# Optimization experiments

Hardware: AMD Instinct MI355X
Metric: run time of the kernel (lower is better)

## Reference

```python
import jax, jax.numpy as jnp
import numpy as np

B, T, D, H = 2, 2048, 1024, 16
DH = D // H


def setup_inputs() -> dict:
    key = jax.random.key(0)
    ks = jax.random.split(key, 5)
    scale = 1.0 / np.sqrt(D)
    return {
        "x": jax.random.normal(ks[0], (B, T, D), dtype=jnp.float32),
        "Wq": jax.random.normal(ks[1], (D, D), dtype=jnp.float32) * scale,
        "Wk": jax.random.normal(ks[2], (D, D), dtype=jnp.float32) * scale,
        "Wv": jax.random.normal(ks[3], (D, D), dtype=jnp.float32) * scale,
        "Wo": jax.random.normal(ks[4], (D, D), dtype=jnp.float32) * scale,
    }


def _split(y):
    # (B,T,D) -> (B,H,T,DH)
    b, t, _ = y.shape
    return y.reshape(b, t, H, DH).transpose(0, 2, 1, 3)


def reference(x, Wq, Wk, Wv, Wo):
    q = _split(x @ Wq)
    k = _split(x @ Wk)
    v = _split(x @ Wv)
    scores = jnp.einsum("bhqd,bhkd->bhqk", q, k) / jnp.sqrt(jnp.float32(DH))
    t = x.shape[1]
    # additive causal mask: -1e9 above the diagonal (matches band_part logic)
    causal = jnp.tril(jnp.ones((t, t), dtype=jnp.float32))
    scores = scores + (1.0 - causal) * -1e9
    attn = jax.nn.softmax(scores, axis=-1)
    out = jnp.einsum("bhqk,bhkd->bhqd", attn, v)  # (B,H,T,DH)
    out = out.transpose(0, 2, 1, 3).reshape(x.shape[0], t, D)
    return out @ Wo
```

## Files before the change

kernel.cpp:

```cpp
#include <hip/hip_runtime.h>

#define BB 2
#define TT 2048
#define DD 1024
#define HH 16
#define DHD 64
#define MM (BB*TT)

typedef __attribute__((ext_vector_type(8))) short short8;
typedef __attribute__((ext_vector_type(4))) float float4v;
typedef unsigned short u16;

__device__ inline float bf2f(u16 u) {
    union { unsigned int i; float f; } v;
    v.i = ((unsigned int)u) << 16;
    return v.f;
}
__device__ inline u16 f2bf(float f) {
    union { float f; unsigned int i; } v;
    v.f = f;
    unsigned int x = v.i;
    unsigned int r = (x + 0x7fffu + ((x >> 16) & 1u)) >> 16;
    return (u16)r;
}

__global__ __launch_bounds__(256) void prep_k(const float* __restrict__ x,
                                              const float* __restrict__ Wq,
                                              const float* __restrict__ Wk,
                                              const float* __restrict__ Wv,
                                              const float* __restrict__ Wo,
                                              u16* __restrict__ xb,
                                              u16* __restrict__ WT) {
    int tid = threadIdx.x;
    if (blockIdx.z == 4) {
        int bid = blockIdx.y * 32 + blockIdx.x;
#pragma unroll
        for (int k = 0; k < 4; k++) {
            int i = bid * 1024 + k * 256 + tid;
            float4v v = ((const float4v*)x)[i];
            ushort4 o;
            o.x = f2bf(v[0]); o.y = f2bf(v[1]); o.z = f2bf(v[2]); o.w = f2bf(v[3]);
            ((ushort4*)xb)[i] = o;
        }
        return;
    }
    __shared__ u16 t[32][33];
    int wsel = blockIdx.z;
    const float* W = (wsel == 0) ? Wq : (wsel == 1) ? Wk : (wsel == 2) ? Wv : Wo;
    u16* o = WT + (size_t)wsel * DD * DD;
    int k0 = blockIdx.y * 32, n0 = blockIdx.x * 32;
    int tx = tid & 31, ty = tid >> 5;
#pragma unroll
    for (int i = 0; i < 4; i++) {
        int k = ty + i * 8;
        t[k][tx] = f2bf(W[(size_t)(k0 + k) * DD + n0 + tx]);
    }
    __syncthreads();
#pragma unroll
    for (int i = 0; i < 4; i++) {
        int n = ty + i * 8;
        o[(size_t)(n0 + n) * DD + k0 + tx] = t[tx][n];
    }
}

template <int MODE, int TM, int TN, int BK>
__global__ __launch_bounds__(256) void gemm_k(const u16* __restrict__ A,
                                              const u16* __restrict__ WT0,
                                              void* __restrict__ outp) {
    const int K = DD;
    const int MT = TM / 32, NT = TN / 32;
    const int NS = (TM + TN) * (BK / 8) / 256;
    const int CPR = BK / 8;

    int z = blockIdx.z;
    const u16* WT = WT0 + (size_t)z * DD * DD;
    int n0 = blockIdx.x * TN, m0 = blockIdx.y * TM;

    __shared__ u16 S[(TM + TN) * BK];

    int tid = threadIdx.x;
    int lane = tid & 63, w = tid >> 6;
    int wm = (w >> 1) * (TM / 2), wn = (w & 1) * (TN / 2);
    int quad = lane >> 4, l16 = lane & 15;

    const u16* gp[NS];
    u16* lp[NS];
#pragma unroll
    for (int j = 0; j < NS; j++) {
        int cid = tid + j * 256;
        int r = cid / CPR, c = cid % CPR;
        lp[j] = S + r * BK + (c ^ (r & 7)) * 8;
        gp[j] = (r < TM ? A + (size_t)(m0 + r) * K
                        : WT + (size_t)(n0 + r - TM) * K) + c * 8;
    }
    int swz = l16 & 7;

    float4v acc[MT][NT];
#pragma unroll
    for (int i = 0; i < MT; i++)
#pragma unroll
        for (int j = 0; j < NT; j++) acc[i][j] = (float4v)(0.0f);

    short8 pr[NS];
#pragma unroll
    for (int j = 0; j < NS; j++) pr[j] = *(const short8*)gp[j];

    const int NK = K / BK;
#pragma unroll 1
    for (int ki = 0; ki < NK; ki++) {
        __syncthreads();
#pragma unroll
        for (int j = 0; j < NS; j++) *(short8*)lp[j] = pr[j];
        __syncthreads();

        if (ki + 1 < NK) {
            int k0 = (ki + 1) * BK;
#pragma unroll
            for (int j = 0; j < NS; j++) pr[j] = *(const short8*)(gp[j] + k0);
        }

#pragma unroll
        for (int ks = 0; ks < BK / 32; ks++) {
            int cq = ((ks * 4 + quad) ^ swz) * 8;
            short8 a[MT], b[NT];
#pragma unroll
            for (int mt = 0; mt < MT; mt++)
                a[mt] = *(const short8*)&S[(wm + mt * 16 + l16) * BK + cq];
#pragma unroll
            for (int nt = 0; nt < NT; nt++)
                b[nt] = *(const short8*)&S[(TM + wn + nt * 16 + l16) * BK + cq];
#pragma unroll
            for (int mt = 0; mt < MT; mt++)
#pragma unroll
                for (int nt = 0; nt < NT; nt++)
                    acc[mt][nt] = __builtin_amdgcn_mfma_f32_16x16x32_bf16(
                        a[mt], b[nt], acc[mt][nt], 0, 0, 0);
        }
    }

#pragma unroll
    for (int mt = 0; mt < MT; mt++) {
#pragma unroll
        for (int nt = 0; nt < NT; nt++) {
#pragma unroll
            for (int r = 0; r < 4; r++) {
                int m = m0 + wm + mt * 16 + quad * 4 + r;
                int n = n0 + wn + nt * 16 + l16;
                float v = acc[mt][nt][r];
                if constexpr (MODE == 0) {
                    int bb = m >> 11, t = m & 2047;
                    int h = n >> 6, dh = n & 63;
                    size_t idx;
                    if (z == 2)
                        idx = (((size_t)2 * BB * HH + bb * HH + h) * DHD + dh) * TT + t;
                    else
                        idx = (((size_t)z * BB * HH + bb * HH + h) * TT + t) * DHD + dh;
                    ((u16*)outp)[idx] = f2bf(v);
                } else {
                    ((float*)outp)[(size_t)m * DD + n] = v;
                }
            }
        }
    }
}

__global__ __launch_bounds__(512) void attn_k(const u16* __restrict__ QKV,
                                              u16* __restrict__ AO) {
    const u16* Q  = QKV;
    const u16* Kp = QKV + (size_t)MM * DD;
    const u16* Vp = QKV + (size_t)2 * MM * DD;
    int bh = blockIdx.y;
    int tswz = (blockIdx.x + blockIdx.y) & 15;
    int p = (blockIdx.y & 16) ? (15 - tswz) : tswz;
    int qA = p, qB = 31 - p;
    size_t hoff = (size_t)bh * TT * DHD;

    __shared__ u16 Qs[2][64 * 64];
    __shared__ u16 Ks[2][64 * 64];
    __shared__ u16 VTs[2][64 * 64];
    __shared__ u16 Ps[8][16 * 64];

    int tid = threadIdx.x;
    int lane = tid & 63, wv = tid >> 6;
    int g = wv >> 2, w4 = wv & 3;
    int quad = lane >> 4, l16 = lane & 15;

    int sr = tid >> 3, sc = tid & 7;
    int sl = sr * 64 + ((sc ^ (sr & 7)) * 8);
    const u16* gK = Kp + hoff + (size_t)sr * DHD + sc * 8;
    const u16* gV = Vp + hoff + (size_t)sr * TT + sc * 8;

    const float qscale = 0.125f * 1.4426950408889634f;
#pragma unroll
    for (int t = 0; t < 2; t++) {
        int q0 = (t ? qB : qA) * 64;
        short8 v = *(const short8*)(Q + hoff + (size_t)(q0 + sr) * DHD + sc * 8);
        short8 sv;
#pragma unroll
        for (int e = 0; e < 8; e++) sv[e] = (short)f2bf(bf2f((u16)v[e]) * qscale);
        *(short8*)&Qs[t][sl] = sv;
    }

    short8 prK = *(const short8*)gK;
    short8 prV = *(const short8*)gV;

    __syncthreads();
    int cxs = l16 & 7;
    int fr = w4 * 16 + l16;
    short8 aq0 = *(const short8*)&Qs[g][fr * 64 + ((quad ^ cxs) * 8)];
    short8 aq1 = *(const short8*)&Qs[g][fr * 64 + (((4 + quad) ^ cxs) * 8)];

    int myqt = g ? qB : qA;
    int ntile = myqt + 1;
    int NR = qB + 1;

    float4v o[4];
#pragma unroll
    for (int i = 0; i < 4; i++) o[i] = (float4v)(0.0f);
    float lr = 0.0f;

#pragma unroll 1
    for (int jt = 0; jt < NR; jt++) {
        int db = jt & 1;
        *(short8*)&Ks[db][sl]  = prK;
        *(short8*)&VTs[db][sl] = prV;
        __syncthreads();

        if (jt + 1 < NR) {
            size_t nj = (size_t)(jt + 1) * 64;
            prK = *(const short8*)(gK + nj * DHD);
            prV = *(const short8*)(gV + nj);
        }

        if (jt < ntile) {
            float4v s[4];
#pragma unroll
            for (int ct = 0; ct < 4; ct++) {
                int kr = (ct * 16 + l16) * 64;
                short8 ak0 = *(const short8*)&Ks[db][kr + ((quad ^ cxs) * 8)];
                short8 ak1 = *(const short8*)&Ks[db][kr + (((4 + quad) ^ cxs) * 8)];
                float4v sv = (float4v)(0.0f);
                sv = __builtin_amdgcn_mfma_f32_16x16x32_bf16(ak0, aq0, sv, 0, 0, 0);
                sv = __builtin_amdgcn_mfma_f32_16x16x32_bf16(ak1, aq1, sv, 0, 0, 0);
                s[ct] = sv;
            }

            if (jt == myqt) {
                int ql = w4 * 16 + l16;
#pragma unroll
                for (int ct = 0; ct < 4; ct++)
#pragma unroll
                    for (int r = 0; r < 4; r++) {
                        int kvl = ct * 16 + quad * 4 + r;
                        if (kvl > ql) s[ct][r] = -30000.0f;
                    }
            }

#pragma unroll
            for (int ct = 0; ct < 4; ct++) {
                float p0 = __builtin_amdgcn_exp2f(s[ct][0]);
                float p1 = __builtin_amdgcn_exp2f(s[ct][1]);
                float p2 = __builtin_amdgcn_exp2f(s[ct][2]);
                float p3 = __builtin_amdgcn_exp2f(s[ct][3]);
                lr += (p0 + p1) + (p2 + p3);
                union { float f; unsigned u; } c0, c1, c2, c3;
                c0.f = p0; c1.f = p1; c2.f = p2; c3.f = p3;
                ushort4 pw;
                pw.x = (u16)(c0.u >> 16);
                pw.y = (u16)(c1.u >> 16);
                pw.z = (u16)(c2.u >> 16);
                pw.w = (u16)(c3.u >> 16);
                int chnk = (ct * 2 + (quad >> 1)) ^ cxs;
                *(ushort4*)&Ps[wv][l16 * 64 + chnk * 8 + (quad & 1) * 4] = pw;
            }

            short8 ap0 = *(const short8*)&Ps[wv][l16 * 64 + ((quad ^ cxs) * 8)];
            short8 ap1 = *(const short8*)&Ps[wv][l16 * 64 + (((4 + quad) ^ cxs) * 8)];
#pragma unroll
            for (int ct = 0; ct < 4; ct++) {
                int vr = (ct * 16 + l16) * 64;
                short8 bv0 = *(const short8*)&VTs[db][vr + ((quad ^ cxs) * 8)];
                short8 bv1 = *(const short8*)&VTs[db][vr + (((4 + quad) ^ cxs) * 8)];
                o[ct] = __builtin_amdgcn_mfma_f32_16x16x32_bf16(ap0, bv0, o[ct], 0, 0, 0);
                o[ct] = __builtin_amdgcn_mfma_f32_16x16x32_bf16(ap1, bv1, o[ct], 0, 0, 0);
            }
        }
    }

    float rs = lr;
    rs += __shfl_xor(rs, 16);
    rs += __shfl_xor(rs, 32);
    int gbase = lane & 48;
    float rinv[4];
#pragma unroll
    for (int r = 0; r < 4; r++)
        rinv[r] = 1.0f / __shfl(rs, gbase + quad * 4 + r);

    int b = bh >> 4, h = bh & 15;
    int q0 = myqt * 64;
#pragma unroll
    for (int ct = 0; ct < 4; ct++) {
#pragma unroll
        for (int r = 0; r < 4; r++) {
            int q = q0 + w4 * 16 + quad * 4 + r;
            int d = h * 64 + ct * 16 + l16;
            AO[(size_t)(b * TT + q) * DD + d] = f2bf(o[ct][r] * rinv[r]);
        }
    }
}

extern "C" void kernel_launch(void* const* d_in, const int* in_sizes, int n_in,
                              void* d_out, int out_size, void* d_ws, size_t ws_size,
                              hipStream_t stream) {
    const float* x  = (const float*)d_in[0];
    const float* Wq = (const float*)d_in[1];
    const float* Wk = (const float*)d_in[2];
    const float* Wv = (const float*)d_in[3];
    const float* Wo = (const float*)d_in[4];

    u16* xb  = (u16*)d_ws;
    u16* WT  = xb + (size_t)MM * DD;
    u16* QKV = WT + (size_t)4 * DD * DD;
    u16* AO  = QKV + (size_t)3 * MM * DD;
    float* out = (float*)d_out;

    prep_k<<<dim3(32, 32, 5), 256, 0, stream>>>(x, Wq, Wk, Wv, Wo, xb, WT);
    gemm_k<0, 128, 128, 64><<<dim3(DD / 128, MM / 128, 3), 256, 0, stream>>>(xb, WT, QKV);
    attn_k<<<dim3(16, 32), 512, 0, stream>>>(QKV, AO);
    gemm_k<1, 64, 128, 128><<<dim3(DD / 128, MM / 64, 1), 256, 0, stream>>>(AO, WT + (size_t)3 * DD * DD, out);
}
```

Measured before the change: 170.4 us.

## Split KV range across wave groups per query tile instead of pairing query tiles

The attention kernel now gives each block a single 64-row query tile. Its two 4-wave groups process alternating KV tiles, loading two KV tiles per iteration, and their partial outputs and row sums are combined through shared memory at the end. This replaces the earlier scheme that paired a short and a long causal query tile per block. The grid doubles to 1024 blocks, ordered longest tile first, to improve load balance and occupancy, at the cost of more LDS and a final reduction step. The output projection GEMM's K tile is also reduced from 128 to 64.

```diff
diff --git a/kernel.cpp b/kernel.cpp
--- a/kernel.cpp
+++ b/kernel.cpp
@@ -169,50 +169,49 @@
     const u16* Q  = QKV;
     const u16* Kp = QKV + (size_t)MM * DD;
     const u16* Vp = QKV + (size_t)2 * MM * DD;
-    int bh = blockIdx.y;
-    int tswz = (blockIdx.x + blockIdx.y) & 15;
-    int p = (blockIdx.y & 16) ? (15 - tswz) : tswz;
-    int qA = p, qB = 31 - p;
+    int bh = blockIdx.x;
+    int qt = 31 - blockIdx.y;
     size_t hoff = (size_t)bh * TT * DHD;
 
-    __shared__ u16 Qs[2][64 * 64];
-    __shared__ u16 Ks[2][64 * 64];
-    __shared__ u16 VTs[2][64 * 64];
+    __shared__ u16 Ks[2][2][64 * 64];
+    __shared__ u16 VTs[2][2][64 * 64];
     __shared__ u16 Ps[8][16 * 64];
 
     int tid = threadIdx.x;
     int lane = tid & 63, wv = tid >> 6;
     int g = wv >> 2, w4 = wv & 3;
     int quad = lane >> 4, l16 = lane & 15;
+    int cxs = l16 & 7;
 
     int sr = tid >> 3, sc = tid & 7;
     int sl = sr * 64 + ((sc ^ (sr & 7)) * 8);
     const u16* gK = Kp + hoff + (size_t)sr * DHD + sc * 8;
     const u16* gV = Vp + hoff + (size_t)sr * TT + sc * 8;
 
+    u16* Qstage = &Ps[0][0];
+
     const float qscale = 0.125f * 1.4426950408889634f;
-#pragma unroll
-    for (int t = 0; t < 2; t++) {
-        int q0 = (t ? qB : qA) * 64;
+    int q0 = qt * 64;
+    {
         short8 v = *(const short8*)(Q + hoff + (size_t)(q0 + sr) * DHD + sc * 8);
         short8 sv;
 #pragma unroll
         for (int e = 0; e < 8; e++) sv[e] = (short)f2bf(bf2f((u16)v[e]) * qscale);
-        *(short8*)&Qs[t][sl] = sv;
-    }
-
-    short8 prK = *(const short8*)gK;
-    short8 prV = *(const short8*)gV;
+        *(short8*)&Qstage[sl] = sv;
+    }
+
+    short8 prK[2], prV[2];
+    prK[0] = *(const short8*)gK;
+    prK[1] = *(const short8*)(gK + (size_t)64 * DHD);
+    prV[0] = *(const short8*)gV;
+    prV[1] = *(const short8*)(gV + 64);
 
     __syncthreads();
-    int cxs = l16 & 7;
     int fr = w4 * 16 + l16;
-    short8 aq0 = *(const short8*)&Qs[g][fr * 64 + ((quad ^ cxs) * 8)];
-    short8 aq1 = *(const short8*)&Qs[g][fr * 64 + (((4 + quad) ^ cxs) * 8)];
-
-    int myqt = g ? qB : qA;
-    int ntile = myqt + 1;
-    int NR = qB + 1;
+    short8 aq0 = *(const short8*)&Qstage[fr * 64 + ((quad ^ cxs) * 8)];
+    short8 aq1 = *(const short8*)&Qstage[fr * 64 + (((4 + quad) ^ cxs) * 8)];
+
+    int NR = (qt >> 1) + 1;
 
     float4v o[4];
 #pragma unroll
@@ -222,30 +221,36 @@
 #pragma unroll 1
     for (int jt = 0; jt < NR; jt++) {
         int db = jt & 1;
-        *(short8*)&Ks[db][sl]  = prK;
-        *(short8*)&VTs[db][sl] = prV;
+#pragma unroll
+        for (int tt = 0; tt < 2; tt++) {
+            *(short8*)&Ks[db][tt][sl]  = prK[tt];
+            *(short8*)&VTs[db][tt][sl] = prV[tt];
+        }
         __syncthreads();
 
         if (jt + 1 < NR) {
-            size_t nj = (size_t)(jt + 1) * 64;
-            prK = *(const short8*)(gK + nj * DHD);
-            prV = *(const short8*)(gV + nj);
-        }
-
-        if (jt < ntile) {
+            size_t nj = (size_t)(jt + 1) * 128;
+            prK[0] = *(const short8*)(gK + nj * DHD);
+            prK[1] = *(const short8*)(gK + (nj + 64) * DHD);
+            prV[0] = *(const short8*)(gV + nj);
+            prV[1] = *(const short8*)(gV + nj + 64);
+        }
+
+        int tj = 2 * jt + g;
+        if (tj <= qt) {
             float4v s[4];
 #pragma unroll
             for (int ct = 0; ct < 4; ct++) {
                 int kr = (ct * 16 + l16) * 64;
-                short8 ak0 = *(const short8*)&Ks[db][kr + ((quad ^ cxs) * 8)];
-                short8 ak1 = *(const short8*)&Ks[db][kr + (((4 + quad) ^ cxs) * 8)];
+                short8 ak0 = *(const short8*)&Ks[db][g][kr + ((quad ^ cxs) * 8)];
+                short8 ak1 = *(const short8*)&Ks[db][g][kr + (((4 + quad) ^ cxs) * 8)];
                 float4v sv = (float4v)(0.0f);
                 sv = __builtin_amdgcn_mfma_f32_16x16x32_bf16(ak0, aq0, sv, 0, 0, 0);
                 sv = __builtin_amdgcn_mfma_f32_16x16x32_bf16(ak1, aq1, sv, 0, 0, 0);
                 s[ct] = sv;
             }
 
-            if (jt == myqt) {
+            if (tj == qt) {
                 int ql = w4 * 16 + l16;
 #pragma unroll
                 for (int ct = 0; ct < 4; ct++)
@@ -279,32 +284,52 @@
 #pragma unroll
             for (int ct = 0; ct < 4; ct++) {
                 int vr = (ct * 16 + l16) * 64;
-                short8 bv0 = *(const short8*)&VTs[db][vr + ((quad ^ cxs) * 8)];
-                short8 bv1 = *(const short8*)&VTs[db][vr + (((4 + quad) ^ cxs) * 8)];
+                short8 bv0 = *(const short8*)&VTs[db][g][vr + ((quad ^ cxs) * 8)];
+                short8 bv1 = *(const short8*)&VTs[db][g][vr + (((4 + quad) ^ cxs) * 8)];
                 o[ct] = __builtin_amdgcn_mfma_f32_16x16x32_bf16(ap0, bv0, o[ct], 0, 0, 0);
                 o[ct] = __builtin_amdgcn_mfma_f32_16x16x32_bf16(ap1, bv1, o[ct], 0, 0, 0);
             }
         }
     }
 
-    float rs = lr;
-    rs += __shfl_xor(rs, 16);
-    rs += __shfl_xor(rs, 32);
-    int gbase = lane & 48;
-    float rinv[4];
-#pragma unroll
-    for (int r = 0; r < 4; r++)
-        rinv[r] = 1.0f / __shfl(rs, gbase + quad * 4 + r);
-
-    int b = bh >> 4, h = bh & 15;
-    int q0 = myqt * 64;
-#pragma unroll
-    for (int ct = 0; ct < 4; ct++) {
-#pragma unroll
-        for (int r = 0; r < 4; r++) {
-            int q = q0 + w4 * 16 + quad * 4 + r;
-            int d = h * 64 + ct * 16 + l16;
-            AO[(size_t)(b * TT + q) * DD + d] = f2bf(o[ct][r] * rinv[r]);
+    __syncthreads();
+    float* Of = (float*)&Ks[0][0][0];
+    float* Lf = (float*)&VTs[0][0][0];
+    if (g == 1) {
+#pragma unroll
+        for (int ct = 0; ct < 4; ct++)
+#pragma unroll
+            for (int r = 0; r < 4; r++)
+                Of[(((w4 * 4 + ct) * 4 + r) * 64) + lane] = o[ct][r];
+        Lf[w4 * 64 + lane] = lr;
+    }
+    __syncthreads();
+    if (g == 0) {
+#pragma unroll
+        for (int ct = 0; ct < 4; ct++)
+#pragma unroll
+            for (int r = 0; r < 4; r++)
+                o[ct][r] += Of[(((w4 * 4 + ct) * 4 + r) * 64) + lane];
+        lr += Lf[w4 * 64 + lane];
+
+        float rs = lr;
+        rs += __shfl_xor(rs, 16);
+        rs += __shfl_xor(rs, 32);
+        int gbase = lane & 48;
+        float rinv[4];
+#pragma unroll
+        for (int r = 0; r < 4; r++)
+            rinv[r] = 1.0f / __shfl(rs, gbase + quad * 4 + r);
+
+        int b = bh >> 4, h = bh & 15;
+#pragma unroll
+        for (int ct = 0; ct < 4; ct++) {
+#pragma unroll
+            for (int r = 0; r < 4; r++) {
+                int q = q0 + w4 * 16 + quad * 4 + r;
+                int d = h * 64 + ct * 16 + l16;
+                AO[(size_t)(b * TT + q) * DD + d] = f2bf(o[ct][r] * rinv[r]);
+            }
         }
     }
 }
@@ -326,6 +351,6 @@
 
     prep_k<<<dim3(32, 32, 5), 256, 0, stream>>>(x, Wq, Wk, Wv, Wo, xb, WT);
     gemm_k<0, 128, 128, 64><<<dim3(DD / 128, MM / 128, 3), 256, 0, stream>>>(xb, WT, QKV);
-    attn_k<<<dim3(16, 32), 512, 0, stream>>>(QKV, AO);
-    gemm_k<1, 64, 128, 128><<<dim3(DD / 128, MM / 64, 1), 256, 0, stream>>>(AO, WT + (size_t)3 * DD * DD, out);
-}
+    attn_k<<<dim3(32, 32), 512, 0, stream>>>(QKV, AO);
+    gemm_k<1, 64, 128, 64><<<dim3(DD / 128, MM / 64, 1), 256, 0, stream>>>(AO, WT + (size_t)3 * DD * DD, out);
+}
```

Measured after the change: 167.0 us. -2.0%, faster.
